# Performance work log

Measured on AMD Instinct MI355X. Metric: run time of the kernel, lower is better.

Reference implementation:

```python
import jax, jax.numpy as jnp
import numpy as np

B, Q, K = 4, 512, 512
QUERY_SIZE = 512
KEY_SIZE = 512
NUM_HIDDENS = 256


def setup_inputs() -> dict:
    key = jax.random.key(0)
    k1, k2, k3, k4, k5 = jax.random.split(key, 5)
    queries = jax.random.normal(k1, (B, Q, 1, QUERY_SIZE), dtype=jnp.float32)
    keys = jax.random.normal(k2, (B, 1, K, KEY_SIZE), dtype=jnp.float32)
    # nn.Linear weights (bias=False); stored as (in, out) for einsum clarity
    W_q = jax.random.normal(k3, (QUERY_SIZE, NUM_HIDDENS), dtype=jnp.float32) * (1.0 / np.sqrt(QUERY_SIZE))
    W_k = jax.random.normal(k4, (KEY_SIZE, NUM_HIDDENS), dtype=jnp.float32) * (1.0 / np.sqrt(KEY_SIZE))
    w_v = jax.random.normal(k5, (NUM_HIDDENS,), dtype=jnp.float32) * (1.0 / np.sqrt(NUM_HIDDENS))
    return {"queries": queries, "keys": keys, "W_q": W_q, "W_k": W_k, "w_v": w_v}


def reference(queries, keys, W_q, W_k, w_v):
    # Project: queries (B,Q,1,Dq) -> (B,Q,1,H); keys (B,1,K,Dk) -> (B,1,K,H)
    q = jnp.einsum('bqod,dh->bqoh', queries, W_q)
    k = jnp.einsum('bokd,dh->bokh', keys, W_k)
    # Broadcast add -> (B,Q,K,H), tanh, reduce hidden via w_v -> (B,Q,K)
    features = jnp.tanh(q + k)
    scores = jnp.einsum('bqkh,h->bqk', features, w_v)
    return scores
```

## Files before the change

### kernel.cpp

```cpp
#include <hip/hip_runtime.h>
#include <hip/hip_bf16.h>

#define HH 256
#define DD 512
#define MM 2048
#define CSCALE 2.8853900817779268f

typedef __bf16 bf16x8 __attribute__((ext_vector_type(8)));
typedef float floatx4 __attribute__((ext_vector_type(4)));

__global__ __launch_bounds__(256) void prep_kernel(
    const float* __restrict__ Wq, const float* __restrict__ Wk,
    const float* __restrict__ wv,
    const float* __restrict__ queries, const float* __restrict__ keys,
    __bf16* __restrict__ Wt, __bf16* __restrict__ Xbf,
    float* __restrict__ wv2, float* __restrict__ sumWp)
{
  const int bx = blockIdx.x;
  if (bx < 256) {
    const int mat  = bx >> 7;
    const int tile = bx & 127;
    const int kt = tile & 15;
    const int nt = tile >> 4;
    const float* __restrict__ W = mat ? Wk : Wq;
    __bf16* __restrict__ Wo = Wt + (size_t)mat * HH * DD;
    __shared__ float lds[32][33];
    const int i = threadIdx.x >> 5;
    const int j = threadIdx.x & 31;
    const int k0 = kt * 32, n0 = nt * 32;
#pragma unroll
    for (int p = 0; p < 4; ++p)
      lds[i + p * 8][j] = W[(k0 + i + p * 8) * HH + n0 + j];
    __syncthreads();
#pragma unroll
    for (int p = 0; p < 4; ++p) {
      const int n = i + p * 8;
      Wo[(n0 + n) * DD + k0 + j] = (__bf16)(lds[j][n] * CSCALE);
    }
  } else if (bx == 256) {
    __shared__ float red[256];
    const int t = threadIdx.x;
    float w = wv[t];
    wv2[t] = -2.0f * w;
    red[t] = w;
    __syncthreads();
    for (int s = 128; s > 0; s >>= 1) {
      if (t < s) red[t] += red[t + s];
      __syncthreads();
    }
    if (t == 0) *sumWp = red[0];
  } else {
    const int blk = bx - 257;
    const size_t dst = (size_t)blk * 2048 + threadIdx.x * 8;
    const float* __restrict__ src =
        (blk < 512) ? (queries + dst) : (keys + dst - (size_t)1048576);
    float4 a = *(const float4*)(src);
    float4 b = *(const float4*)(src + 4);
    bf16x8 v;
    v[0] = (__bf16)a.x; v[1] = (__bf16)a.y; v[2] = (__bf16)a.z; v[3] = (__bf16)a.w;
    v[4] = (__bf16)b.x; v[5] = (__bf16)b.y; v[6] = (__bf16)b.z; v[7] = (__bf16)b.w;
    *(bf16x8*)(Xbf + dst) = v;
  }
}

__global__ __launch_bounds__(256, 4) void proj_kernel(
    const __bf16* __restrict__ Xbf, const __bf16* __restrict__ Wt,
    float* __restrict__ eqp, __bf16* __restrict__ ekb)
{
  const int w    = threadIdx.x >> 6;
  const int lane = threadIdx.x & 63;
  const int quad = lane >> 4;
  const int r    = lane & 15;
  const int tw = w & 1;
  const int ks = w >> 1;
  const bool is_k = (blockIdx.z != 0);
  const __bf16* __restrict__ X  = Xbf + (is_k ? (size_t)1048576 : 0);
  const __bf16* __restrict__ Wb = Wt + (is_k ? (size_t)HH * DD : 0);

  const int m0 = blockIdx.x * 32 + tw * 16;
  const int n0 = blockIdx.y * 32;

  floatx4 acc0 = {0.f, 0.f, 0.f, 0.f};
  floatx4 acc1 = {0.f, 0.f, 0.f, 0.f};
  const __bf16* arow = X + (size_t)(m0 + r) * DD + ks * 256 + quad * 8;
  const __bf16* b0   = Wb + (size_t)(n0 + r) * DD + ks * 256 + quad * 8;
  const __bf16* b1   = b0 + 16 * DD;

#pragma unroll
  for (int kk = 0; kk < 256; kk += 32) {
    bf16x8 af  = *(const bf16x8*)(arow + kk);
    bf16x8 bf0 = *(const bf16x8*)(b0 + kk);
    bf16x8 bf1 = *(const bf16x8*)(b1 + kk);
    acc0 = __builtin_amdgcn_mfma_f32_16x16x32_bf16(af, bf0, acc0, 0, 0, 0);
    acc1 = __builtin_amdgcn_mfma_f32_16x16x32_bf16(af, bf1, acc1, 0, 0, 0);
  }

  __shared__ float part[2][64][9];
  if (ks == 1) {
#pragma unroll
    for (int i = 0; i < 4; ++i) {
      part[tw][lane][i]     = acc0[i];
      part[tw][lane][4 + i] = acc1[i];
    }
  }
  __syncthreads();
  if (ks == 0) {
#pragma unroll
    for (int i = 0; i < 4; ++i) {
      acc0[i] += part[tw][lane][i];
      acc1[i] += part[tw][lane][4 + i];
    }
    const int mrow = m0 + quad * 4;
    if (!is_k) {
#pragma unroll
      for (int i = 0; i < 4; ++i) {
        eqp[(size_t)(mrow + i) * HH + n0 + r] =
            __builtin_amdgcn_exp2f(acc0[i]);
        eqp[(size_t)(mrow + i) * HH + n0 + 16 + r] =
            __builtin_amdgcn_exp2f(acc1[i]);
      }
    } else {
      const int na = n0 + r, nb = n0 + 16 + r;
#pragma unroll
      for (int i = 0; i < 4; ++i) {
        ekb[((size_t)(na >> 2) * MM + (mrow + i)) * 4 + (na & 3)] =
            (__bf16)__builtin_amdgcn_exp2f(acc0[i]);
        ekb[((size_t)(nb >> 2) * MM + (mrow + i)) * 4 + (nb & 3)] =
            (__bf16)__builtin_amdgcn_exp2f(acc1[i]);
      }
    }
  }
}

__device__ __forceinline__ float quad_term(
    float ek0, float ek1, float ek2, float ek3,
    float4 e, float4 w, float acc)
{
  float u0 = fmaf(e.x, ek0, 1.0f);
  float u1 = fmaf(e.y, ek1, 1.0f);
  float u2 = fmaf(e.z, ek2, 1.0f);
  float u3 = fmaf(e.w, ek3, 1.0f);
  float p01 = u0 * u1;
  float p23 = u2 * u3;
  float n01 = fmaf(w.y, u0, w.x * u1);
  float n23 = fmaf(w.w, u2, w.z * u3);
  float N   = fmaf(n23, p01, n01 * p23);
  float r   = __builtin_amdgcn_rcpf(p01 * p23);
  return fmaf(N, r, acc);
}

__global__ __launch_bounds__(256, 8) void score_kernel(
    const float* __restrict__ eqp, const uint2* __restrict__ ekb,
    const float* __restrict__ wv2, const float* __restrict__ sumWp,
    float* __restrict__ out)
{
  __shared__ __align__(16) float eqs[2][256];
  __shared__ __align__(16) float wvs[256];

  const int t  = threadIdx.x;
  const int b  = blockIdx.z;
  const int k  = blockIdx.x * 256 + t;
  const int q0 = blockIdx.y * 2;

  {
    const float2* __restrict__ src =
        (const float2*)(eqp + (size_t)(b * 512 + q0) * HH);
    ((float2*)eqs)[t] = src[t];
    wvs[t] = wv2[t];
  }
  const float sumW = *sumWp;
  __syncthreads();

  const uint2* __restrict__ kptr = ekb + (size_t)b * 512 + k;

  float acc0 = 0.f, acc1 = 0.f;

#pragma unroll 2
  for (int hq = 0; hq < 64; ++hq) {
    uint2 kp = kptr[(size_t)hq * MM];
    float4 e0 = *(const float4*)&eqs[0][hq * 4];
    float4 e1 = *(const float4*)&eqs[1][hq * 4];
    float4 w4 = *(const float4*)&wvs[hq * 4];
    float ek0 = __uint_as_float(kp.x << 16);
    float ek1 = __uint_as_float(kp.x & 0xffff0000u);
    float ek2 = __uint_as_float(kp.y << 16);
    float ek3 = __uint_as_float(kp.y & 0xffff0000u);
    acc0 = quad_term(ek0, ek1, ek2, ek3, e0, w4, acc0);
    acc1 = quad_term(ek0, ek1, ek2, ek3, e1, w4, acc1);
  }

  const size_t ob = ((size_t)(b * 512 + q0)) * 512 + blockIdx.x * 256 + t;
  out[ob]       = sumW + acc0;
  out[ob + 512] = sumW + acc1;
}

extern "C" void kernel_launch(void* const* d_in, const int* in_sizes, int n_in,
                              void* d_out, int out_size, void* d_ws, size_t ws_size,
                              hipStream_t stream) {
  (void)in_sizes; (void)n_in; (void)out_size; (void)ws_size;
  const float* queries = (const float*)d_in[0];
  const float* Keys    = (const float*)d_in[1];
  const float* Wq      = (const float*)d_in[2];
  const float* Wk      = (const float*)d_in[3];
  const float* wv      = (const float*)d_in[4];
  float* out = (float*)d_out;

  char* ws = (char*)d_ws;
  __bf16* Wt    = (__bf16*)ws;
  float*  wv2   = (float*)(ws + (512 << 10));
  float*  sumWp = (float*)(ws + (513 << 10));
  __bf16* Xbf   = (__bf16*)(ws + (1 << 20));
  float*  eqp   = (float*)(ws + (5ull << 20));
  __bf16* ekb   = (__bf16*)(ws + (7ull << 20));

  prep_kernel<<<dim3(1281), 256, 0, stream>>>(
      Wq, Wk, wv, queries, Keys, Wt, Xbf, wv2, sumWp);
  proj_kernel<<<dim3(64, 8, 2), 256, 0, stream>>>(Xbf, Wt, eqp, ekb);
  score_kernel<<<dim3(2, 256, 4), 256, 0, stream>>>(
      eqp, (const uint2*)ekb, wv2, sumWp, out);
}
```

Before: 112.9 us.

## Split hidden dimension across blocks, register-block four queries, atomically combine partial scores

The score kernel now has each thread compute four queries instead of two, reusing each loaded key vector across more query rows. The hidden dimension is split into two halves handled by separate blocks, and their partial sums are combined with atomic adds into an output that is memset to zero first. This is meant to cut global key traffic per output and raise arithmetic intensity. The cost is an extra memset, atomic output traffic, and a dependence on out_size being an element count.

```diff
diff --git a/kernel.cpp b/kernel.cpp
--- a/kernel.cpp
+++ b/kernel.cpp
@@ -154,50 +154,63 @@
     const float* __restrict__ wv2, const float* __restrict__ sumWp,
     float* __restrict__ out)
 {
-  __shared__ __align__(16) float eqs[2][256];
-  __shared__ __align__(16) float wvs[256];
+  __shared__ __align__(16) float eqs[4][128];
+  __shared__ __align__(16) float wvs[128];
 
   const int t  = threadIdx.x;
   const int b  = blockIdx.z;
   const int k  = blockIdx.x * 256 + t;
-  const int q0 = blockIdx.y * 2;
+  const int qt = blockIdx.y >> 1;
+  const int hb = blockIdx.y & 1;
+  const int q0 = qt * 4;
 
   {
-    const float2* __restrict__ src =
-        (const float2*)(eqp + (size_t)(b * 512 + q0) * HH);
-    ((float2*)eqs)[t] = src[t];
-    wvs[t] = wv2[t];
-  }
-  const float sumW = *sumWp;
+    int idx0 = t, idx1 = t + 256;
+    eqs[idx0 >> 7][idx0 & 127] =
+        eqp[(size_t)(b * 512 + q0 + (idx0 >> 7)) * HH + hb * 128 + (idx0 & 127)];
+    eqs[idx1 >> 7][idx1 & 127] =
+        eqp[(size_t)(b * 512 + q0 + (idx1 >> 7)) * HH + hb * 128 + (idx1 & 127)];
+    if (t < 128) wvs[t] = wv2[hb * 128 + t];
+  }
+  const float sumW = (hb == 0) ? *sumWp : 0.0f;
   __syncthreads();
 
-  const uint2* __restrict__ kptr = ekb + (size_t)b * 512 + k;
-
-  float acc0 = 0.f, acc1 = 0.f;
-
-#pragma unroll 2
-  for (int hq = 0; hq < 64; ++hq) {
-    uint2 kp = kptr[(size_t)hq * MM];
-    float4 e0 = *(const float4*)&eqs[0][hq * 4];
-    float4 e1 = *(const float4*)&eqs[1][hq * 4];
-    float4 w4 = *(const float4*)&wvs[hq * 4];
-    float ek0 = __uint_as_float(kp.x << 16);
-    float ek1 = __uint_as_float(kp.x & 0xffff0000u);
-    float ek2 = __uint_as_float(kp.y << 16);
-    float ek3 = __uint_as_float(kp.y & 0xffff0000u);
-    acc0 = quad_term(ek0, ek1, ek2, ek3, e0, w4, acc0);
-    acc1 = quad_term(ek0, ek1, ek2, ek3, e1, w4, acc1);
-  }
-
-  const size_t ob = ((size_t)(b * 512 + q0)) * 512 + blockIdx.x * 256 + t;
-  out[ob]       = sumW + acc0;
-  out[ob + 512] = sumW + acc1;
+  const uint2* __restrict__ kptr =
+      ekb + (size_t)(hb * 32) * MM + (size_t)b * 512 + k;
+
+  float acc0 = 0.f, acc1 = 0.f, acc2 = 0.f, acc3 = 0.f;
+
+  for (int c = 0; c < 8; ++c) {
+    uint2 kb[4];
+#pragma unroll
+    for (int i = 0; i < 4; ++i)
+      kb[i] = kptr[(size_t)(c * 4 + i) * MM];
+#pragma unroll
+    for (int i = 0; i < 4; ++i) {
+      const int hq = c * 4 + i;
+      float ek0 = __uint_as_float(kb[i].x << 16);
+      float ek1 = __uint_as_float(kb[i].x & 0xffff0000u);
+      float ek2 = __uint_as_float(kb[i].y << 16);
+      float ek3 = __uint_as_float(kb[i].y & 0xffff0000u);
+      float4 w4 = *(const float4*)&wvs[hq * 4];
+      acc0 = quad_term(ek0, ek1, ek2, ek3, *(const float4*)&eqs[0][hq * 4], w4, acc0);
+      acc1 = quad_term(ek0, ek1, ek2, ek3, *(const float4*)&eqs[1][hq * 4], w4, acc1);
+      acc2 = quad_term(ek0, ek1, ek2, ek3, *(const float4*)&eqs[2][hq * 4], w4, acc2);
+      acc3 = quad_term(ek0, ek1, ek2, ek3, *(const float4*)&eqs[3][hq * 4], w4, acc3);
+    }
+  }
+
+  float* obase = out + ((size_t)(b * 512 + q0)) * 512 + blockIdx.x * 256 + t;
+  unsafeAtomicAdd(obase,        sumW + acc0);
+  unsafeAtomicAdd(obase + 512,  sumW + acc1);
+  unsafeAtomicAdd(obase + 1024, sumW + acc2);
+  unsafeAtomicAdd(obase + 1536, sumW + acc3);
 }
 
 extern "C" void kernel_launch(void* const* d_in, const int* in_sizes, int n_in,
                               void* d_out, int out_size, void* d_ws, size_t ws_size,
                               hipStream_t stream) {
-  (void)in_sizes; (void)n_in; (void)out_size; (void)ws_size;
+  (void)in_sizes; (void)n_in; (void)ws_size;
   const float* queries = (const float*)d_in[0];
   const float* Keys    = (const float*)d_in[1];
   const float* Wq      = (const float*)d_in[2];
@@ -213,6 +226,8 @@
   float*  eqp   = (float*)(ws + (5ull << 20));
   __bf16* ekb   = (__bf16*)(ws + (7ull << 20));
 
+  hipMemsetAsync(d_out, 0, (size_t)out_size * sizeof(float), stream);
+
   prep_kernel<<<dim3(1281), 256, 0, stream>>>(
       Wq, Wk, wv, queries, Keys, Wt, Xbf, wv2, sumWp);
   proj_kernel<<<dim3(64, 8, 2), 256, 0, stream>>>(Xbf, Wt, eqp, ekb);
```

Result: slower. 175.0 us (+55.0%).
